# Performance work log

Hardware: AMD Instinct MI355X
Metric: run time of the kernel (lower is better)

## Reference

```python
import jax, jax.numpy as jnp
import numpy as np

N_NODES = 100000
N_EDGES = 800000
DIM = 128
BN_EPS = 1e-5


def setup_inputs() -> dict:
    key = jax.random.key(0)
    k1, k2, k3 = jax.random.split(key, 3)
    x = jax.random.normal(k1, (N_NODES, DIM), dtype=jnp.float32)
    edge_index = jax.random.randint(k2, (2, N_EDGES), 0, N_NODES, dtype=jnp.int64)
    # xavier-uniform-like init for the linear weight [out, in]
    limit = float(np.sqrt(6.0 / (DIM + DIM)))
    W = jax.random.uniform(k3, (DIM, DIM), dtype=jnp.float32, minval=-limit, maxval=limit)
    bias = jnp.zeros((DIM,), dtype=jnp.float32)
    bn_gamma = jnp.ones((DIM,), dtype=jnp.float32)
    bn_beta = jnp.zeros((DIM,), dtype=jnp.float32)
    return {"x": x, "edge_index": edge_index, "W": W, "bias": bias,
            "bn_gamma": bn_gamma, "bn_beta": bn_beta, "bit_sum": 0}


def reference(x, edge_index, W, bias, bn_gamma, bn_beta, bit_sum):
    n = x.shape[0]
    # Linear (no bias), is_q=False path; q_xw treated as identity.
    h = x @ W.T                                   # [N, D]
    row, col = edge_index[0], edge_index[1]
    # symmetric degree normalization: deg computed over destination (col)
    deg = jax.ops.segment_sum(jnp.ones_like(col, dtype=h.dtype), col, num_segments=n)
    deg_inv_sqrt = jnp.where(deg > 0, jax.lax.rsqrt(jnp.maximum(deg, 1.0)), 0.0)
    norm = deg_inv_sqrt[row] * deg_inv_sqrt[col]  # [E]
    # message: norm * x_j (x_j = h[row]), aggregate (add) at col
    msg = norm[:, None] * h[row]                  # [E, D]
    out = jax.ops.segment_sum(msg, col, num_segments=n)  # [N, D]
    out = out + bias
    # BatchNorm1d (training mode: batch stats, biased variance)
    mean = jnp.mean(out, axis=0)
    var = jnp.var(out, axis=0)
    out = (out - mean) * jax.lax.rsqrt(var + BN_EPS) * bn_gamma + bn_beta
    # activation
    out = jax.nn.relu(out)
    # residual (in_dim == out_dim); dropout p=0 -> identity
    out = out + x
    return (out, 0)
```

## Files before the change

kernel.cpp:

```cpp
#include <hip/hip_runtime.h>
#include <cstddef>

#define NN 100000
#define DD 128
#define ND (NN * DD)
#define BN_EPS 1e-5f
#define LDA 136
#define NREP 64
#define NBKT 98
#define EPB 4096

typedef __bf16 bf16_t;
typedef bf16_t bf16x8 __attribute__((ext_vector_type(8)));
typedef float f32x4 __attribute__((ext_vector_type(4)));
typedef unsigned int uint;
typedef unsigned short ushort;


__device__ __forceinline__ ushort f2b(float f) {
    uint u = __builtin_bit_cast(uint, f);
    u += 0x7FFFu + ((u >> 16) & 1u);
    return (ushort)(u >> 16);
}
__device__ __forceinline__ float b2f(uint s) {
    return __builtin_bit_cast(float, s << 16);
}

__device__ __forceinline__ int detect_i64(const int* __restrict__ ei) {
    __shared__ int sflag;
    int t = threadIdx.x;
    if (t < 64) {
        int hi = ei[2 * t + 1];
        unsigned long long b = __ballot(hi == 0);
        if (t == 0) sflag = (b == ~0ull) ? 1 : 0;
    }
    __syncthreads();
    return sflag;
}

__global__ __launch_bounds__(256) void k_pack(const float* __restrict__ x,
                                              uint* __restrict__ xb,
                                              const float* __restrict__ W,
                                              uint* __restrict__ wb) {
    int i = blockIdx.x * 256 + threadIdx.x;
    const float* src;
    uint* dst;
    int j;
    if (i < ND / 8) { src = x; dst = xb; j = i; }
    else { j = i - ND / 8; if (j >= (DD * DD) / 8) return; src = W; dst = wb; }
    const float4* s4 = (const float4*)src;
    float4 a = s4[2 * j], b = s4[2 * j + 1];
    uint4 o;
    o.x = (uint)f2b(a.x) | ((uint)f2b(a.y) << 16);
    o.y = (uint)f2b(a.z) | ((uint)f2b(a.w) << 16);
    o.z = (uint)f2b(b.x) | ((uint)f2b(b.y) << 16);
    o.w = (uint)f2b(b.z) | ((uint)f2b(b.w) << 16);
    ((uint4*)dst)[j] = o;
}

__global__ __launch_bounds__(256) void k_bcnt(const int* __restrict__ ei,
                                              int* __restrict__ bktot, int E) {
    int f = detect_i64(ei);
    __shared__ int hist[NBKT];
    int t = threadIdx.x;
    if (t < NBKT) hist[t] = 0;
    __syncthreads();
    int base = blockIdx.x * EPB;
    int count = min(EPB, E - base);
    for (int i = t; i < count; i += 256) {
        int e = base + i;
        int c = f ? ei[2 * (E + e)] : ei[E + e];
        atomicAdd(&hist[c >> 10], 1);
    }
    __syncthreads();
    if (t < NBKT && hist[t] > 0) atomicAdd(&bktot[t], hist[t]);
}

__global__ void k_bscan(const int* __restrict__ bktot, int* __restrict__ bbase,
                        int* __restrict__ bcur, int E) {
    int t = threadIdx.x;
    __shared__ int ls[NBKT];
    if (t < NBKT) ls[t] = bktot[t];
    __syncthreads();
    if (t == 0) {
        int run = 0;
        for (int i = 0; i < NBKT; ++i) { int v = ls[i]; ls[i] = run; run += v; }
    }
    __syncthreads();
    if (t < NBKT) { bbase[t] = ls[t]; bcur[t] = ls[t]; }
    if (t == 0) bbase[NBKT] = E;
}

__global__ __launch_bounds__(256) void k_bin(const int* __restrict__ ei,
                                             int* __restrict__ bcur,
                                             uint2* __restrict__ pairs, int E) {
    int f = detect_i64(ei);
    __shared__ int hist[NBKT], scur[NBKT];
    int t = threadIdx.x;
    if (t < NBKT) hist[t] = 0;
    __syncthreads();
    int base = blockIdx.x * EPB;
    int count = min(EPB, E - base);
    int rr[16], cc[16];
#pragma unroll
    for (int k = 0; k < 16; ++k) {
        int i = t + k * 256;
        if (i < count) {
            int e = base + i;
            int r, c;
            if (f) { r = ei[2 * e]; c = ei[2 * (E + e)]; }
            else   { r = ei[e];     c = ei[E + e]; }
            rr[k] = r; cc[k] = c;
            atomicAdd(&hist[c >> 10], 1);
        }
    }
    __syncthreads();
    if (t < NBKT) scur[t] = atomicAdd(&bcur[t], hist[t]);
    __syncthreads();
#pragma unroll
    for (int k = 0; k < 16; ++k) {
        int i = t + k * 256;
        if (i < count) {
            int b = cc[k] >> 10;
            int pos = atomicAdd(&scur[b], 1);
            pairs[pos] = (uint2){(uint)rr[k], (uint)cc[k]};
        }
    }
}

__global__ __launch_bounds__(256) void k_cnt(const uint2* __restrict__ pairs,
                                             const int* __restrict__ bbase,
                                             int* __restrict__ ptr0,
                                             int* __restrict__ cnt,
                                             float* __restrict__ dinv,
                                             int* __restrict__ srow) {
    __shared__ int hist[1024];
    __shared__ int scur[1024];
    __shared__ int ls[256];
    int b = blockIdx.x;
    int t = threadIdx.x;
    int e0 = bbase[b], e1 = bbase[b + 1];
    int nodebase = b << 10;
#pragma unroll
    for (int i = 0; i < 4; ++i) hist[t + i * 256] = 0;
    __syncthreads();
    for (int i = e0 + t; i < e1; i += 256)
        atomicAdd(&hist[(int)pairs[i].y - nodebase], 1);
    __syncthreads();
    int c4[4];
    int lsum = 0;
#pragma unroll
    for (int i = 0; i < 4; ++i) { c4[i] = hist[t * 4 + i]; lsum += c4[i]; }
    ls[t] = lsum;
    __syncthreads();
    for (int o = 1; o < 256; o <<= 1) {
        int v = (t >= o) ? ls[t - o] : 0;
        __syncthreads();
        ls[t] += v;
        __syncthreads();
    }
    int run = ls[t] - lsum + e0;
#pragma unroll
    for (int i = 0; i < 4; ++i) {
        int idx = nodebase + t * 4 + i;
        if (idx < NN) {
            ptr0[idx] = run;
            cnt[idx] = c4[i];
            dinv[idx] = c4[i] > 0 ? rsqrtf((float)c4[i]) : 0.f;
        }
        scur[t * 4 + i] = run;
        run += c4[i];
    }
    __syncthreads();
    for (int i = e0 + t; i < e1; i += 256) {
        uint2 p = pairs[i];
        int pos = atomicAdd(&scur[(int)p.y - nodebase], 1);
        srow[pos] = (int)p.x;
    }
}

__global__ __launch_bounds__(256) void k_gather(const uint* __restrict__ xb,
                                                const int* __restrict__ srow,
                                                const int* __restrict__ ptr0,
                                                const int* __restrict__ cnt,
                                                const float* __restrict__ dinv,
                                                uint* __restrict__ aggb) {
    int n = blockIdx.x * 4 + (threadIdx.x >> 6);
    int lane = threadIdx.x & 63;
    int s = ptr0[n];
    int k = cnt[n];
    float dc = dinv[n];
    float ax = 0.f, ay = 0.f;
    for (int base = 0; base < k; base += 64) {
        int m = min(k - base, 64);
        int rj = 0; float wj = 0.f;
        if (lane < m) { rj = srow[s + base + lane]; wj = dinv[rj]; }
        int j = 0;
        for (; j + 4 <= m; j += 4) {
            int r0 = __shfl(rj, j);     float w0 = __shfl(wj, j);
            int r1 = __shfl(rj, j + 1); float w1 = __shfl(wj, j + 1);
            int r2 = __shfl(rj, j + 2); float w2 = __shfl(wj, j + 2);
            int r3 = __shfl(rj, j + 3); float w3 = __shfl(wj, j + 3);
            uint v0 = xb[(size_t)r0 * 64 + lane];
            uint v1 = xb[(size_t)r1 * 64 + lane];
            uint v2 = xb[(size_t)r2 * 64 + lane];
            uint v3 = xb[(size_t)r3 * 64 + lane];
            ax = fmaf(w0, b2f(v0 & 0xFFFFu), ax); ay = fmaf(w0, b2f(v0 >> 16), ay);
            ax = fmaf(w1, b2f(v1 & 0xFFFFu), ax); ay = fmaf(w1, b2f(v1 >> 16), ay);
            ax = fmaf(w2, b2f(v2 & 0xFFFFu), ax); ay = fmaf(w2, b2f(v2 >> 16), ay);
            ax = fmaf(w3, b2f(v3 & 0xFFFFu), ax); ay = fmaf(w3, b2f(v3 >> 16), ay);
        }
        for (; j < m; ++j) {
            int r = __shfl(rj, j);
            float w = __shfl(wj, j);
            uint v = xb[(size_t)r * 64 + lane];
            ax = fmaf(w, b2f(v & 0xFFFFu), ax);
            ay = fmaf(w, b2f(v >> 16), ay);
        }
    }
    aggb[(size_t)n * 64 + lane] = (uint)f2b(dc * ax) | ((uint)f2b(dc * ay) << 16);
}

__global__ __launch_bounds__(256, 2) void k_gemm(const ushort* __restrict__ aggb,
                                                 const ushort* __restrict__ wb,
                                                 ushort* __restrict__ hb,
                                                 float* __restrict__ csr,
                                                 float* __restrict__ cqr) {
    __shared__ ushort sA[64 * LDA];
    __shared__ float cp[4][128], cq[4][128];
    int t = threadIdx.x;
    int wave = t >> 6, lane = t & 63;
    int quad = lane >> 4, l16 = lane & 15;
    size_t rowbase = (size_t)blockIdx.x * 64;

    bf16x8 Bf[8][4];
#pragma unroll
    for (int ct = 0; ct < 8; ++ct)
#pragma unroll
        for (int ks = 0; ks < 4; ++ks) {
            const uint4* p =
                (const uint4*)(wb + (size_t)(ct * 16 + l16) * 128 + ks * 32 + quad * 8);
            Bf[ct][ks] = __builtin_bit_cast(bf16x8, *p);
        }

#pragma unroll
    for (int i = 0; i < 4; ++i) {
        int c = t + i * 256;
        int r = c >> 4, pos = c & 15;
        size_t gr = rowbase + r;
        uint4 v = {0u, 0u, 0u, 0u};
        if (gr < NN) v = *(const uint4*)(aggb + gr * 128 + pos * 8);
        *(uint4*)(sA + r * LDA + pos * 8) = v;
    }
    __syncthreads();

    bf16x8 Af[4];
#pragma unroll
    for (int ks = 0; ks < 4; ++ks)
        Af[ks] = __builtin_bit_cast(
            bf16x8, *(const uint4*)(sA + (wave * 16 + l16) * LDA + ks * 32 + quad * 8));

    f32x4 acc[8];
#pragma unroll
    for (int ct = 0; ct < 8; ++ct) {
        acc[ct] = (f32x4){0.f, 0.f, 0.f, 0.f};
#pragma unroll
        for (int ks = 0; ks < 4; ++ks)
            acc[ct] = __builtin_amdgcn_mfma_f32_16x16x32_bf16(Af[ks], Bf[ct][ks],
                                                              acc[ct], 0, 0, 0);
    }

#pragma unroll
    for (int ct = 0; ct < 8; ++ct) {
        float ss = 0.f, qq = 0.f;
#pragma unroll
        for (int r = 0; r < 4; ++r) {
            float v = acc[ct][r];
            ss += v; qq += v * v;
            size_t row = rowbase + wave * 16 + quad * 4 + r;
            if (row < NN) hb[row * 128 + ct * 16 + l16] = f2b(v);
        }
        ss += __shfl_xor(ss, 16); ss += __shfl_xor(ss, 32);
        qq += __shfl_xor(qq, 16); qq += __shfl_xor(qq, 32);
        if (quad == 0) { cp[wave][ct * 16 + l16] = ss; cq[wave][ct * 16 + l16] = qq; }
    }
    __syncthreads();
    if (t < 128) {
        int rep = (blockIdx.x & (NREP - 1)) * 128 + t;
        atomicAdd(&csr[rep], cp[0][t] + cp[1][t] + cp[2][t] + cp[3][t]);
        atomicAdd(&cqr[rep], cq[0][t] + cq[1][t] + cq[2][t] + cq[3][t]);
    }
}

__global__ void k_red(const float* __restrict__ csr, const float* __restrict__ cqr,
                      float* __restrict__ colsum, float* __restrict__ colsumsq) {
    int t = threadIdx.x;
    if (t < 128) {
        float s = 0.f;
        for (int i = 0; i < NREP; ++i) s += csr[i * 128 + t];
        colsum[t] = s;
    } else {
        int c = t - 128;
        float s = 0.f;
        for (int i = 0; i < NREP; ++i) s += cqr[i * 128 + c];
        colsumsq[c] = s;
    }
}

__global__ __launch_bounds__(256) void k_final(const uint* __restrict__ hb,
                                               const uint* __restrict__ xb,
                                               const float* __restrict__ gamma,
                                               const float* __restrict__ beta,
                                               const float* __restrict__ colsum,
                                               const float* __restrict__ colsumsq,
                                               float* __restrict__ out, int out_size) {
    int gid = blockIdx.x * 256 + threadIdx.x;
    int c4 = (gid & 31) * 4;
    uint2 hv = ((const uint2*)hb)[gid];
    uint2 xv = ((const uint2*)xb)[gid];
    float hval[4] = { b2f(hv.x & 0xFFFFu), b2f(hv.x >> 16),
                      b2f(hv.y & 0xFFFFu), b2f(hv.y >> 16) };
    float xval[4] = { b2f(xv.x & 0xFFFFu), b2f(xv.x >> 16),
                      b2f(xv.y & 0xFFFFu), b2f(xv.y >> 16) };
    const float invN = 1.0f / NN;
    float4 o;
    float res[4];
#pragma unroll
    for (int j = 0; j < 4; ++j) {
        float m = colsum[c4 + j] * invN;
        float var = colsumsq[c4 + j] * invN - m * m;
        float inv = rsqrtf(var + BN_EPS);
        float val = (hval[j] - m) * inv * gamma[c4 + j] + beta[c4 + j];
        res[j] = fmaxf(val, 0.f) + xval[j];
    }
    o.x = res[0]; o.y = res[1]; o.z = res[2]; o.w = res[3];
    ((float4*)out)[gid] = o;
    if (gid == 0 && out_size > ND) out[ND] = 0.0f;
}

extern "C" void kernel_launch(void* const* d_in, const int* in_sizes, int n_in,
                              void* d_out, int out_size, void* d_ws, size_t ws_size,
                              hipStream_t stream) {
    const float* x     = (const float*)d_in[0];
    const int*   ei    = (const int*)d_in[1];
    const float* W     = (const float*)d_in[2];
    const float* gamma = (const float*)d_in[4];
    const float* beta  = (const float*)d_in[5];
    float* ws = (float*)d_ws;
    float* out = (float*)d_out;

    uint*   hb       = (uint*)ws;
    uint*   xb       = hb + ND / 2;
    uint*   aggb     = xb + ND / 2;
    float*  csr      = (float*)(aggb + ND / 2);
    float*  cqr      = csr + NREP * 128;
    int*    bktot    = (int*)(cqr + NREP * 128);
    int*    cnt      = bktot + 128;
    int*    bbase    = cnt + NN;
    int*    bcur     = bbase + 128;
    float*  colsum   = (float*)(bcur + 128);
    float*  colsumsq = colsum + 128;
    int*    ptr0     = (int*)(colsumsq + 128);
    float*  dinv     = (float*)(ptr0 + NN);
    int*    srow     = (int*)(dinv + NN);

    int E = in_sizes[1] / 2;
    uint* wb = (uint*)(srow + E);

    uint2* pairs = (uint2*)hb;

    int nbc = (ND / 8 + (DD * DD) / 8 + 255) / 256;
    int nbin = (E + EPB - 1) / EPB;

    hipMemsetAsync(csr, 0, (size_t)(2 * NREP * 128 + 128) * 4, stream);
    k_bcnt<<<nbin, 256, 0, stream>>>(ei, bktot, E);
    k_pack<<<nbc, 256, 0, stream>>>(x, xb, W, wb);
    k_bscan<<<1, 128, 0, stream>>>(bktot, bbase, bcur, E);
    k_bin<<<nbin, 256, 0, stream>>>(ei, bcur, pairs, E);
    k_cnt<<<NBKT, 256, 0, stream>>>(pairs, bbase, ptr0, cnt, dinv, srow);
    k_gather<<<NN / 4, 256, 0, stream>>>(xb, srow, ptr0, cnt, dinv, aggb);
    k_gemm<<<(NN + 63) / 64, 256, 0, stream>>>((const ushort*)aggb, (const ushort*)wb,
                                               (ushort*)hb, csr, cqr);
    k_red<<<1, 256, 0, stream>>>(csr, cqr, colsum, colsumsq);
    k_final<<<ND / (256 * 4), 256, 0, stream>>>(hb, xb, gamma, beta,
                                                colsum, colsumsq, out, out_size);
}
```

Measured before the change: 249.4 us.

## Fuse gather with GEMM, merge prep kernels, and fold scan/reduction into consumers

Merges the bucket-count and pack kernels into one launch, folds the bucket prefix scan into k_bin and k_cnt, fuses the neighbor gather directly into the MFMA GEMM via shared memory (dropping the aggb round-trip), and folds the column-stat reduction into the final kernel with wider vectorized stores. It also cuts the number of partial-stat replicas from 64 to 16 and loads W fragments per column tile rather than holding all of them in registers. This removes several launches and an intermediate buffer write and read, but each block now repeats the scan and reduction work, and gather latency is serialized ahead of the GEMM within a block.

Result: faster. 230.8 us (-7.5%).

```diff
diff --git a/kernel.cpp b/kernel.cpp
--- a/kernel.cpp
+++ b/kernel.cpp
@@ -6,7 +6,7 @@
 #define ND (NN * DD)
 #define BN_EPS 1e-5f
 #define LDA 136
-#define NREP 64
+#define NREP 16
 #define NBKT 98
 #define EPB 4096
 
@@ -38,11 +38,30 @@
     return sflag;
 }
 
-__global__ __launch_bounds__(256) void k_pack(const float* __restrict__ x,
+__global__ __launch_bounds__(256) void k_prep(const int* __restrict__ ei,
+                                              int* __restrict__ bktot, int E, int nbh,
+                                              const float* __restrict__ x,
                                               uint* __restrict__ xb,
                                               const float* __restrict__ W,
                                               uint* __restrict__ wb) {
-    int i = blockIdx.x * 256 + threadIdx.x;
+    if ((int)blockIdx.x < nbh) {
+        int f = detect_i64(ei);
+        __shared__ int hist[NBKT];
+        int t = threadIdx.x;
+        if (t < NBKT) hist[t] = 0;
+        __syncthreads();
+        int base = blockIdx.x * EPB;
+        int count = min(EPB, E - base);
+        for (int i = t; i < count; i += 256) {
+            int e = base + i;
+            int c = f ? ei[2 * (E + e)] : ei[E + e];
+            atomicAdd(&hist[c >> 10], 1);
+        }
+        __syncthreads();
+        if (t < NBKT && hist[t] > 0) atomicAdd(&bktot[t], hist[t]);
+        return;
+    }
+    int i = (blockIdx.x - nbh) * 256 + threadIdx.x;
     const float* src;
     uint* dst;
     int j;
@@ -58,47 +77,19 @@
     ((uint4*)dst)[j] = o;
 }
 
-__global__ __launch_bounds__(256) void k_bcnt(const int* __restrict__ ei,
-                                              int* __restrict__ bktot, int E) {
-    int f = detect_i64(ei);
-    __shared__ int hist[NBKT];
-    int t = threadIdx.x;
-    if (t < NBKT) hist[t] = 0;
-    __syncthreads();
-    int base = blockIdx.x * EPB;
-    int count = min(EPB, E - base);
-    for (int i = t; i < count; i += 256) {
-        int e = base + i;
-        int c = f ? ei[2 * (E + e)] : ei[E + e];
-        atomicAdd(&hist[c >> 10], 1);
-    }
-    __syncthreads();
-    if (t < NBKT && hist[t] > 0) atomicAdd(&bktot[t], hist[t]);
-}
-
-__global__ void k_bscan(const int* __restrict__ bktot, int* __restrict__ bbase,
-                        int* __restrict__ bcur, int E) {
-    int t = threadIdx.x;
-    __shared__ int ls[NBKT];
-    if (t < NBKT) ls[t] = bktot[t];
-    __syncthreads();
-    if (t == 0) {
-        int run = 0;
-        for (int i = 0; i < NBKT; ++i) { int v = ls[i]; ls[i] = run; run += v; }
-    }
-    __syncthreads();
-    if (t < NBKT) { bbase[t] = ls[t]; bcur[t] = ls[t]; }
-    if (t == 0) bbase[NBKT] = E;
-}
-
 __global__ __launch_bounds__(256) void k_bin(const int* __restrict__ ei,
+                                             const int* __restrict__ bktot,
                                              int* __restrict__ bcur,
                                              uint2* __restrict__ pairs, int E) {
     int f = detect_i64(ei);
-    __shared__ int hist[NBKT], scur[NBKT];
-    int t = threadIdx.x;
-    if (t < NBKT) hist[t] = 0;
-    __syncthreads();
+    __shared__ int bb[NBKT], hist[NBKT], scur[NBKT];
+    int t = threadIdx.x;
+    if (t < NBKT) { bb[t] = bktot[t]; hist[t] = 0; }
+    __syncthreads();
+    if (t == 0) {
+        int run = 0;
+        for (int i = 0; i < NBKT; ++i) { int v = bb[i]; bb[i] = run; run += v; }
+    }
     int base = blockIdx.x * EPB;
     int count = min(EPB, E - base);
     int rr[16], cc[16];
@@ -115,7 +106,7 @@
         }
     }
     __syncthreads();
-    if (t < NBKT) scur[t] = atomicAdd(&bcur[t], hist[t]);
+    if (t < NBKT) scur[t] = bb[t] + atomicAdd(&bcur[t], hist[t]);
     __syncthreads();
 #pragma unroll
     for (int k = 0; k < 16; ++k) {
@@ -129,7 +120,7 @@
 }
 
 __global__ __launch_bounds__(256) void k_cnt(const uint2* __restrict__ pairs,
-                                             const int* __restrict__ bbase,
+                                             const int* __restrict__ bktot,
                                              int* __restrict__ ptr0,
                                              int* __restrict__ cnt,
                                              float* __restrict__ dinv,
@@ -137,13 +128,22 @@
     __shared__ int hist[1024];
     __shared__ int scur[1024];
     __shared__ int ls[256];
+    __shared__ int bb[NBKT];
+    __shared__ int se0, se1;
     int b = blockIdx.x;
     int t = threadIdx.x;
-    int e0 = bbase[b], e1 = bbase[b + 1];
+    if (t < NBKT) bb[t] = bktot[t];
+#pragma unroll
+    for (int i = 0; i < 4; ++i) hist[t + i * 256] = 0;
+    __syncthreads();
+    if (t == 0) {
+        int run = 0;
+        for (int i = 0; i < b; ++i) run += bb[i];
+        se0 = run; se1 = run + bb[b];
+    }
+    __syncthreads();
+    int e0 = se0, e1 = se1;
     int nodebase = b << 10;
-#pragma unroll
-    for (int i = 0; i < 4; ++i) hist[t + i * 256] = 0;
-    __syncthreads();
     for (int i = e0 + t; i < e1; i += 256)
         atomicAdd(&hist[(int)pairs[i].y - nodebase], 1);
     __syncthreads();
@@ -179,103 +179,111 @@
     }
 }
 
-__global__ __launch_bounds__(256) void k_gather(const uint* __restrict__ xb,
-                                                const int* __restrict__ srow,
-                                                const int* __restrict__ ptr0,
-                                                const int* __restrict__ cnt,
-                                                const float* __restrict__ dinv,
-                                                uint* __restrict__ aggb) {
-    int n = blockIdx.x * 4 + (threadIdx.x >> 6);
-    int lane = threadIdx.x & 63;
-    int s = ptr0[n];
-    int k = cnt[n];
-    float dc = dinv[n];
-    float ax = 0.f, ay = 0.f;
-    for (int base = 0; base < k; base += 64) {
-        int m = min(k - base, 64);
-        int rj = 0; float wj = 0.f;
-        if (lane < m) { rj = srow[s + base + lane]; wj = dinv[rj]; }
-        int j = 0;
-        for (; j + 4 <= m; j += 4) {
-            int r0 = __shfl(rj, j);     float w0 = __shfl(wj, j);
-            int r1 = __shfl(rj, j + 1); float w1 = __shfl(wj, j + 1);
-            int r2 = __shfl(rj, j + 2); float w2 = __shfl(wj, j + 2);
-            int r3 = __shfl(rj, j + 3); float w3 = __shfl(wj, j + 3);
-            uint v0 = xb[(size_t)r0 * 64 + lane];
-            uint v1 = xb[(size_t)r1 * 64 + lane];
-            uint v2 = xb[(size_t)r2 * 64 + lane];
-            uint v3 = xb[(size_t)r3 * 64 + lane];
-            ax = fmaf(w0, b2f(v0 & 0xFFFFu), ax); ay = fmaf(w0, b2f(v0 >> 16), ay);
-            ax = fmaf(w1, b2f(v1 & 0xFFFFu), ax); ay = fmaf(w1, b2f(v1 >> 16), ay);
-            ax = fmaf(w2, b2f(v2 & 0xFFFFu), ax); ay = fmaf(w2, b2f(v2 >> 16), ay);
-            ax = fmaf(w3, b2f(v3 & 0xFFFFu), ax); ay = fmaf(w3, b2f(v3 >> 16), ay);
-        }
-        for (; j < m; ++j) {
-            int r = __shfl(rj, j);
-            float w = __shfl(wj, j);
-            uint v = xb[(size_t)r * 64 + lane];
-            ax = fmaf(w, b2f(v & 0xFFFFu), ax);
-            ay = fmaf(w, b2f(v >> 16), ay);
-        }
-    }
-    aggb[(size_t)n * 64 + lane] = (uint)f2b(dc * ax) | ((uint)f2b(dc * ay) << 16);
-}
-
-__global__ __launch_bounds__(256, 2) void k_gemm(const ushort* __restrict__ aggb,
-                                                 const ushort* __restrict__ wb,
-                                                 ushort* __restrict__ hb,
-                                                 float* __restrict__ csr,
-                                                 float* __restrict__ cqr) {
+__global__ __launch_bounds__(256, 4) void k_gg(const uint* __restrict__ xb,
+                                               const int* __restrict__ srow,
+                                               const int* __restrict__ ptr0,
+                                               const int* __restrict__ cnt,
+                                               const float* __restrict__ dinv,
+                                               const ushort* __restrict__ wb,
+                                               ushort* __restrict__ hb,
+                                               float* __restrict__ csr,
+                                               float* __restrict__ cqr) {
     __shared__ ushort sA[64 * LDA];
     __shared__ float cp[4][128], cq[4][128];
     int t = threadIdx.x;
     int wave = t >> 6, lane = t & 63;
+    size_t rowbase = (size_t)blockIdx.x * 64;
+
+    int mn = (int)rowbase + wave * 16 + (lane & 15);
+    int sv = 0, kv = 0;
+    float dv = 0.f;
+    if (lane < 16 && mn < NN) { sv = ptr0[mn]; kv = cnt[mn]; dv = dinv[mn]; }
+    for (int i = 0; i < 16; ++i) {
+        int s = __shfl(sv, i);
+        int k = __shfl(kv, i);
+        float dc = __shfl(dv, i);
+        float ax = 0.f, ay = 0.f;
+        for (int base = 0; base < k; base += 64) {
+            int m = min(k - base, 64);
+            int rj = 0; float wj = 0.f;
+            if (lane < m) { rj = srow[s + base + lane]; wj = dinv[rj]; }
+            int j = 0;
+            for (; j + 8 <= m; j += 8) {
+                int r0 = __shfl(rj, j);     float w0 = __shfl(wj, j);
+                int r1 = __shfl(rj, j + 1); float w1 = __shfl(wj, j + 1);
+                int r2 = __shfl(rj, j + 2); float w2 = __shfl(wj, j + 2);
+                int r3 = __shfl(rj, j + 3); float w3 = __shfl(wj, j + 3);
+                int r4 = __shfl(rj, j + 4); float w4 = __shfl(wj, j + 4);
+                int r5 = __shfl(rj, j + 5); float w5 = __shfl(wj, j + 5);
+                int r6 = __shfl(rj, j + 6); float w6 = __shfl(wj, j + 6);
+                int r7 = __shfl(rj, j + 7); float w7 = __shfl(wj, j + 7);
+                uint v0 = xb[(size_t)r0 * 64 + lane];
+                uint v1 = xb[(size_t)r1 * 64 + lane];
+                uint v2 = xb[(size_t)r2 * 64 + lane];
+                uint v3 = xb[(size_t)r3 * 64 + lane];
+                uint v4 = xb[(size_t)r4 * 64 + lane];
+                uint v5 = xb[(size_t)r5 * 64 + lane];
+                uint v6 = xb[(size_t)r6 * 64 + lane];
+                uint v7 = xb[(size_t)r7 * 64 + lane];
+                ax = fmaf(w0, b2f(v0 & 0xFFFFu), ax); ay = fmaf(w0, b2f(v0 >> 16), ay);
+                ax = fmaf(w1, b2f(v1 & 0xFFFFu), ax); ay = fmaf(w1, b2f(v1 >> 16), ay);
+                ax = fmaf(w2, b2f(v2 & 0xFFFFu), ax); ay = fmaf(w2, b2f(v2 >> 16), ay);
+                ax = fmaf(w3, b2f(v3 & 0xFFFFu), ax); ay = fmaf(w3, b2f(v3 >> 16), ay);
+                ax = fmaf(w4, b2f(v4 & 0xFFFFu), ax); ay = fmaf(w4, b2f(v4 >> 16), ay);
+                ax = fmaf(w5, b2f(v5 & 0xFFFFu), ax); ay = fmaf(w5, b2f(v5 >> 16), ay);
+                ax = fmaf(w6, b2f(v6 & 0xFFFFu), ax); ay = fmaf(w6, b2f(v6 >> 16), ay);
+                ax = fmaf(w7, b2f(v7 & 0xFFFFu), ax); ay = fmaf(w7, b2f(v7 >> 16), ay);
+            }
+            for (; j + 4 <= m; j += 4) {
+                int r0 = __shfl(rj, j);     float w0 = __shfl(wj, j);
+                int r1 = __shfl(rj, j + 1); float w1 = __shfl(wj, j + 1);
+                int r2 = __shfl(rj, j + 2); float w2 = __shfl(wj, j + 2);
+                int r3 = __shfl(rj, j + 3); float w3 = __shfl(wj, j + 3);
+                uint v0 = xb[(size_t)r0 * 64 + lane];
+                uint v1 = xb[(size_t)r1 * 64 + lane];
+                uint v2 = xb[(size_t)r2 * 64 + lane];
+                uint v3 = xb[(size_t)r3 * 64 + lane];
+                ax = fmaf(w0, b2f(v0 & 0xFFFFu), ax); ay = fmaf(w0, b2f(v0 >> 16), ay);
+                ax = fmaf(w1, b2f(v1 & 0xFFFFu), ax); ay = fmaf(w1, b2f(v1 >> 16), ay);
+                ax = fmaf(w2, b2f(v2 & 0xFFFFu), ax); ay = fmaf(w2, b2f(v2 >> 16), ay);
+                ax = fmaf(w3, b2f(v3 & 0xFFFFu), ax); ay = fmaf(w3, b2f(v3 >> 16), ay);
+            }
+            for (; j < m; ++j) {
+                int r = __shfl(rj, j);
+                float w = __shfl(wj, j);
+                uint v = xb[(size_t)r * 64 + lane];
+                ax = fmaf(w, b2f(v & 0xFFFFu), ax);
+                ay = fmaf(w, b2f(v >> 16), ay);
+            }
+        }
+        uint o = (uint)f2b(dc * ax) | ((uint)f2b(dc * ay) << 16);
+        *(uint*)(sA + (wave * 16 + i) * LDA + lane * 2) = o;
+    }
+    __syncthreads();
+
     int quad = lane >> 4, l16 = lane & 15;
-    size_t rowbase = (size_t)blockIdx.x * 64;
-
-    bf16x8 Bf[8][4];
-#pragma unroll
-    for (int ct = 0; ct < 8; ++ct)
-#pragma unroll
-        for (int ks = 0; ks < 4; ++ks) {
-            const uint4* p =
-                (const uint4*)(wb + (size_t)(ct * 16 + l16) * 128 + ks * 32 + quad * 8);
-            Bf[ct][ks] = __builtin_bit_cast(bf16x8, *p);
-        }
-
-#pragma unroll
-    for (int i = 0; i < 4; ++i) {
-        int c = t + i * 256;
-        int r = c >> 4, pos = c & 15;
-        size_t gr = rowbase + r;
-        uint4 v = {0u, 0u, 0u, 0u};
-        if (gr < NN) v = *(const uint4*)(aggb + gr * 128 + pos * 8);
-        *(uint4*)(sA + r * LDA + pos * 8) = v;
-    }
-    __syncthreads();
-
     bf16x8 Af[4];
 #pragma unroll
     for (int ks = 0; ks < 4; ++ks)
         Af[ks] = __builtin_bit_cast(
             bf16x8, *(const uint4*)(sA + (wave * 16 + l16) * LDA + ks * 32 + quad * 8));
 
-    f32x4 acc[8];
 #pragma unroll
     for (int ct = 0; ct < 8; ++ct) {
-        acc[ct] = (f32x4){0.f, 0.f, 0.f, 0.f};
+        bf16x8 Bf[4];
 #pragma unroll
         for (int ks = 0; ks < 4; ++ks)
-            acc[ct] = __builtin_amdgcn_mfma_f32_16x16x32_bf16(Af[ks], Bf[ct][ks],
-                                                              acc[ct], 0, 0, 0);
-    }
-
-#pragma unroll
-    for (int ct = 0; ct < 8; ++ct) {
+            Bf[ks] = __builtin_bit_cast(
+                bf16x8,
+                *(const uint4*)(wb + (size_t)(ct * 16 + l16) * 128 + ks * 32 + quad * 8));
+        f32x4 acc = (f32x4){0.f, 0.f, 0.f, 0.f};
+#pragma unroll
+        for (int ks = 0; ks < 4; ++ks)
+            acc = __builtin_amdgcn_mfma_f32_16x16x32_bf16(Af[ks], Bf[ks], acc, 0, 0, 0);
         float ss = 0.f, qq = 0.f;
 #pragma unroll
         for (int r = 0; r < 4; ++r) {
-            float v = acc[ct][r];
+            float v = acc[r];
             ss += v; qq += v * v;
             size_t row = rowbase + wave * 16 + quad * 4 + r;
             if (row < NN) hb[row * 128 + ct * 16 + l16] = f2b(v);
@@ -292,50 +300,58 @@
     }
 }
 
-__global__ void k_red(const float* __restrict__ csr, const float* __restrict__ cqr,
-                      float* __restrict__ colsum, float* __restrict__ colsumsq) {
-    int t = threadIdx.x;
+__global__ __launch_bounds__(256) void k_final(const uint* __restrict__ hb,
+                                               const uint* __restrict__ xb,
+                                               const float* __restrict__ gamma,
+                                               const float* __restrict__ beta,
+                                               const float* __restrict__ csr,
+                                               const float* __restrict__ cqr,
+                                               float* __restrict__ out, int out_size) {
+    __shared__ float sa[128], sb[128];
+    int t = threadIdx.x;
+    const float invN = 1.0f / NN;
     if (t < 128) {
         float s = 0.f;
         for (int i = 0; i < NREP; ++i) s += csr[i * 128 + t];
-        colsum[t] = s;
+        sa[t] = s * invN;
     } else {
         int c = t - 128;
         float s = 0.f;
         for (int i = 0; i < NREP; ++i) s += cqr[i * 128 + c];
-        colsumsq[c] = s;
-    }
-}
-
-__global__ __launch_bounds__(256) void k_final(const uint* __restrict__ hb,
-                                               const uint* __restrict__ xb,
-                                               const float* __restrict__ gamma,
-                                               const float* __restrict__ beta,
-                                               const float* __restrict__ colsum,
-                                               const float* __restrict__ colsumsq,
-                                               float* __restrict__ out, int out_size) {
-    int gid = blockIdx.x * 256 + threadIdx.x;
-    int c4 = (gid & 31) * 4;
-    uint2 hv = ((const uint2*)hb)[gid];
-    uint2 xv = ((const uint2*)xb)[gid];
-    float hval[4] = { b2f(hv.x & 0xFFFFu), b2f(hv.x >> 16),
-                      b2f(hv.y & 0xFFFFu), b2f(hv.y >> 16) };
-    float xval[4] = { b2f(xv.x & 0xFFFFu), b2f(xv.x >> 16),
-                      b2f(xv.y & 0xFFFFu), b2f(xv.y >> 16) };
-    const float invN = 1.0f / NN;
-    float4 o;
-    float res[4];
-#pragma unroll
-    for (int j = 0; j < 4; ++j) {
-        float m = colsum[c4 + j] * invN;
-        float var = colsumsq[c4 + j] * invN - m * m;
+        sb[c] = s * invN;
+    }
+    __syncthreads();
+    if (t < 128) {
+        float m = sa[t];
+        float var = sb[t] - m * m;
         float inv = rsqrtf(var + BN_EPS);
-        float val = (hval[j] - m) * inv * gamma[c4 + j] + beta[c4 + j];
-        res[j] = fmaxf(val, 0.f) + xval[j];
-    }
-    o.x = res[0]; o.y = res[1]; o.z = res[2]; o.w = res[3];
-    ((float4*)out)[gid] = o;
-    if (gid == 0 && out_size > ND) out[ND] = 0.0f;
+        float A = inv * gamma[t];
+        float B = beta[t] - m * A;
+        sa[t] = A; sb[t] = B;
+    }
+    __syncthreads();
+
+    int c0 = (t & 7) * 16;
+    int u8 = blockIdx.x * 512 + t * 2;
+    uint4 hv0 = ((const uint4*)hb)[u8], hv1 = ((const uint4*)hb)[u8 + 1];
+    uint4 xv0 = ((const uint4*)xb)[u8], xv1 = ((const uint4*)xb)[u8 + 1];
+    uint hu[8] = {hv0.x, hv0.y, hv0.z, hv0.w, hv1.x, hv1.y, hv1.z, hv1.w};
+    uint xu[8] = {xv0.x, xv0.y, xv0.z, xv0.w, xv1.x, xv1.y, xv1.z, xv1.w};
+    float res[16];
+#pragma unroll
+    for (int p = 0; p < 8; ++p) {
+        int c = c0 + p * 2;
+        float h0 = b2f(hu[p] & 0xFFFFu), h1 = b2f(hu[p] >> 16);
+        float x0 = b2f(xu[p] & 0xFFFFu), x1 = b2f(xu[p] >> 16);
+        res[2 * p]     = fmaxf(fmaf(h0, sa[c],     sb[c]),     0.f) + x0;
+        res[2 * p + 1] = fmaxf(fmaf(h1, sa[c + 1], sb[c + 1]), 0.f) + x1;
+    }
+    float4* o4 = (float4*)out;
+    int ob = blockIdx.x * 1024 + t * 4;
+#pragma unroll
+    for (int q = 0; q < 4; ++q)
+        o4[ob + q] = (float4){res[4 * q], res[4 * q + 1], res[4 * q + 2], res[4 * q + 3]};
+    if (blockIdx.x == 0 && t == 0 && out_size > ND) out[ND] = 0.0f;
 }
 
 extern "C" void kernel_launch(void* const* d_in, const int* in_sizes, int n_in,
@@ -351,16 +367,12 @@
 
     uint*   hb       = (uint*)ws;
     uint*   xb       = hb + ND / 2;
-    uint*   aggb     = xb + ND / 2;
-    float*  csr      = (float*)(aggb + ND / 2);
+    float*  csr      = (float*)(xb + ND / 2);
     float*  cqr      = csr + NREP * 128;
     int*    bktot    = (int*)(cqr + NREP * 128);
-    int*    cnt      = bktot + 128;
-    int*    bbase    = cnt + NN;
-    int*    bcur     = bbase + 128;
-    float*  colsum   = (float*)(bcur + 128);
-    float*  colsumsq = colsum + 128;
-    int*    ptr0     = (int*)(colsumsq + 128);
+    int*    bcur     = bktot + 128;
+    int*    cnt      = bcur + 128;
+    int*    ptr0     = cnt + NN;
     float*  dinv     = (float*)(ptr0 + NN);
     int*    srow     = (int*)(dinv + NN);
 
@@ -372,16 +384,12 @@
     int nbc = (ND / 8 + (DD * DD) / 8 + 255) / 256;
     int nbin = (E + EPB - 1) / EPB;
 
-    hipMemsetAsync(csr, 0, (size_t)(2 * NREP * 128 + 128) * 4, stream);
-    k_bcnt<<<nbin, 256, 0, stream>>>(ei, bktot, E);
-    k_pack<<<nbc, 256, 0, stream>>>(x, xb, W, wb);
-    k_bscan<<<1, 128, 0, stream>>>(bktot, bbase, bcur, E);
-    k_bin<<<nbin, 256, 0, stream>>>(ei, bcur, pairs, E);
-    k_cnt<<<NBKT, 256, 0, stream>>>(pairs, bbase, ptr0, cnt, dinv, srow);
-    k_gather<<<NN / 4, 256, 0, stream>>>(xb, srow, ptr0, cnt, dinv, aggb);
-    k_gemm<<<(NN + 63) / 64, 256, 0, stream>>>((const ushort*)aggb, (const ushort*)wb,
-                                               (ushort*)hb, csr, cqr);
-    k_red<<<1, 256, 0, stream>>>(csr, cqr, colsum, colsumsq);
-    k_final<<<ND / (256 * 4), 256, 0, stream>>>(hb, xb, gamma, beta,
-                                                colsum, colsumsq, out, out_size);
-}
+    hipMemsetAsync(csr, 0, (size_t)(2 * NREP * 128 + 256) * 4, stream);
+    k_prep<<<nbin + nbc, 256, 0, stream>>>(ei, bktot, E, nbin, x, xb, W, wb);
+    k_bin<<<nbin, 256, 0, stream>>>(ei, bktot, bcur, pairs, E);
+    k_cnt<<<NBKT, 256, 0, stream>>>(pairs, bktot, ptr0, cnt, dinv, srow);
+    k_gg<<<(NN + 63) / 64, 256, 0, stream>>>(xb, srow, ptr0, cnt, dinv,
+                                             (const ushort*)wb, (ushort*)hb, csr, cqr);
+    k_final<<<ND / 4096, 256, 0, stream>>>(hb, xb, gamma, beta, csr, cqr,
+                                           out, out_size);
+}
```
